# Performance work log

Hardware: AMD Instinct MI355X
Metric: run time of the kernel (lower is better)

Reference implementation:

```python
import jax, jax.numpy as jnp
import numpy as np

# Layered DAG: NIN input neurons, L topological batches of B neurons each,
# each batch fully connected (via mask) to the previous batch.
L, B, NIN = 16, 2048, 2048
N = NIN + L * B  # total neurons = 34816


def setup_inputs() -> dict:
    key = jax.random.key(0)
    k1, k2, k3 = jax.random.split(key, 3)
    x = jax.random.normal(k1, (NIN,), jnp.float32)
    # per-topo-batch weight matrices [L, B, B], scaled like standard init
    weights = jax.random.normal(k2, (L, B, B), jnp.float32) / np.sqrt(B).astype(np.float32)
    # dense connectivity masks (structural; all ones for a layered net)
    masks = jnp.ones((L, B, B), jnp.float32)
    biases = jax.random.normal(k3, (L, B), jnp.float32) * 0.01
    # global ids of each batch's predecessor neurons: batch l reads [l*B, (l+1)*B)
    indices = jnp.arange(L * B, dtype=jnp.int32).reshape(L, B)
    # global ids of the neurons in each topo batch (offset by the input neurons)
    tb = indices + NIN
    return {"x": x, "weights": weights, "masks": masks, "biases": biases,
            "indices": indices, "tb": tb}


def reference(x, weights, masks, biases, indices, tb):
    # values: flat per-neuron activation buffer, inputs written first
    values = jnp.zeros((N,), dtype=x.dtype).at[jnp.arange(NIN)].set(x)
    # last topo batch = output neurons -> identity activation; others -> silu
    is_output = jnp.arange(L) == L - 1

    def step(values, batch):
        W, M, idx, t, b, is_out = batch
        vals = values[idx]                      # gather predecessor values [B]
        affine = (W * M) @ vals + b             # masked weighted sum [B]
        out = jnp.where(is_out, affine, jax.nn.silu(affine))
        return values.at[t].set(out), None      # scatter back

    values, _ = jax.lax.scan(step, values, (weights, masks, indices, tb, biases, is_output))
    # output_transform = identity; read output neurons in order
    return values[tb[-1]]
```

## Files before the change

### kernel.cpp

```cpp
#include <hip/hip_runtime.h>
#include <math.h>


#define LB 2048
#define NL 16

__global__ __launch_bounds__(256) void gemv_act(
    const float* __restrict__ W,
    const float* __restrict__ bias,
    const float* __restrict__ vin,
    float* __restrict__ vout,
    int apply_silu)
{
    const int lane = threadIdx.x & 63;
    const int row  = (blockIdx.x * blockDim.x + threadIdx.x) >> 6;

    const float4* __restrict__ Wrow = (const float4*)(W + (size_t)row * LB);
    const float4* __restrict__ v4   = (const float4*)vin;

    float acc = 0.f;
#pragma unroll
    for (int it = 0; it < (LB / 4) / 64; ++it) {
        const int j = it * 64 + lane;
        float4 w = Wrow[j];
        float4 v = v4[j];
        acc += w.x * v.x + w.y * v.y + w.z * v.z + w.w * v.w;
    }

#pragma unroll
    for (int off = 32; off > 0; off >>= 1)
        acc += __shfl_down(acc, off, 64);

    if (lane == 0) {
        float y = acc + bias[row];
        if (apply_silu) y = y / (1.f + expf(-y));
        vout[row] = y;
    }
}

extern "C" void kernel_launch(void* const* d_in, const int* in_sizes, int n_in,
                              void* d_out, int out_size, void* d_ws, size_t ws_size,
                              hipStream_t stream)
{
    const float* x       = (const float*)d_in[0];
    const float* weights = (const float*)d_in[1];
    const float* biases  = (const float*)d_in[3];
    float* out = (float*)d_out;

    float* buf0 = (float*)d_ws;
    float* buf1 = buf0 + LB;

    const float* cur = x;
    for (int l = 0; l < NL; ++l) {
        const int is_last = (l == NL - 1);
        float* next = is_last ? out : ((l & 1) ? buf1 : buf0);
        gemv_act<<<LB / 4, 256, 0, stream>>>(
            weights + (size_t)l * LB * LB,
            biases  + (size_t)l * LB,
            cur, next, !is_last);
        cur = next;
    }
}
```

Before: 495.2 us.

## Fuse all layers into one cooperative kernel with grid-wide sync

Replaces sixteen per-layer GEMV launches with a single cooperative kernel that loops over layers and calls grid.sync between them. This is meant to remove per-launch overhead and inter-kernel gaps. In exchange it adds sixteen grid barriers, and it requires all 512 blocks to be co-resident, which launch bounds of two blocks per CU aim to guarantee.

```diff
diff --git a/kernel.cpp b/kernel.cpp
--- a/kernel.cpp
+++ b/kernel.cpp
@@ -1,40 +1,56 @@
 #include <hip/hip_runtime.h>
+#include <hip/hip_cooperative_groups.h>
 #include <math.h>
+
+namespace cg = cooperative_groups;
 
 
 #define LB 2048
 #define NL 16
 
-__global__ __launch_bounds__(256) void gemv_act(
+__global__ __launch_bounds__(256, 2) void fused_mlp(
     const float* __restrict__ W,
     const float* __restrict__ bias,
-    const float* __restrict__ vin,
-    float* __restrict__ vout,
-    int apply_silu)
+    const float* __restrict__ x,
+    float* __restrict__ out,
+    float* __restrict__ buf0,
+    float* __restrict__ buf1)
 {
+    cg::grid_group grid = cg::this_grid();
+
     const int lane = threadIdx.x & 63;
-    const int row  = (blockIdx.x * blockDim.x + threadIdx.x) >> 6;
+    const int row  = (int)((blockIdx.x * blockDim.x + threadIdx.x) >> 6);
 
-    const float4* __restrict__ Wrow = (const float4*)(W + (size_t)row * LB);
-    const float4* __restrict__ v4   = (const float4*)vin;
+    const float* cur = x;
+#pragma unroll 1
+    for (int l = 0; l < NL; ++l) {
+        float* next = (l == NL - 1) ? out : ((l & 1) ? buf1 : buf0);
 
-    float acc = 0.f;
+        const float4* __restrict__ Wrow =
+            (const float4*)(W + ((size_t)l * LB + row) * LB);
+        const float4* __restrict__ v4 = (const float4*)cur;
+
+        float acc = 0.f;
 #pragma unroll
-    for (int it = 0; it < (LB / 4) / 64; ++it) {
-        const int j = it * 64 + lane;
-        float4 w = Wrow[j];
-        float4 v = v4[j];
-        acc += w.x * v.x + w.y * v.y + w.z * v.z + w.w * v.w;
-    }
+        for (int it = 0; it < (LB / 4) / 64; ++it) {
+            const int j = it * 64 + lane;
+            float4 w = Wrow[j];
+            float4 v = v4[j];
+            acc += w.x * v.x + w.y * v.y + w.z * v.z + w.w * v.w;
+        }
 
 #pragma unroll
-    for (int off = 32; off > 0; off >>= 1)
-        acc += __shfl_down(acc, off, 64);
+        for (int off = 32; off > 0; off >>= 1)
+            acc += __shfl_down(acc, off, 64);
 
-    if (lane == 0) {
-        float y = acc + bias[row];
-        if (apply_silu) y = y / (1.f + expf(-y));
-        vout[row] = y;
+        if (lane == 0) {
+            float y = acc + bias[l * LB + row];
+            if (l != NL - 1) y = y / (1.f + expf(-y));
+            next[row] = y;
+        }
+
+        grid.sync();
+        cur = next;
     }
 }
 
@@ -45,19 +61,12 @@
     const float* x       = (const float*)d_in[0];
     const float* weights = (const float*)d_in[1];
     const float* biases  = (const float*)d_in[3];
-    float* out = (float*)d_out;
-
+    float* out  = (float*)d_out;
     float* buf0 = (float*)d_ws;
     float* buf1 = buf0 + LB;
 
-    const float* cur = x;
-    for (int l = 0; l < NL; ++l) {
-        const int is_last = (l == NL - 1);
-        float* next = is_last ? out : ((l & 1) ? buf1 : buf0);
-        gemv_act<<<LB / 4, 256, 0, stream>>>(
-            weights + (size_t)l * LB * LB,
-            biases  + (size_t)l * LB,
-            cur, next, !is_last);
-        cur = next;
-    }
+    void* args[] = {(void*)&weights, (void*)&biases, (void*)&x,
+                    (void*)&out, (void*)&buf0, (void*)&buf1};
+    hipLaunchCooperativeKernel((void*)fused_mlp, dim3(512), dim3(256),
+                               args, 0, stream);
 }
```

New measurement: 1.251 ms. +152.7%, slower.
